# Kernel optimization log

Measured on AMD Instinct MI355X. Metric: run time of the kernel, lower is better.

The kernel has to match this reference:

```python
import jax, jax.numpy as jnp
import numpy as np

N_NODES = 100000
N_EDGES = 3200000
N_FEAT = 256
N_CLASS = 4


def setup_inputs() -> dict:
    key = jax.random.key(0)
    ks = jax.random.split(key, 8)
    x = jax.random.normal(ks[0], (N_NODES, N_FEAT), dtype=jnp.float32)
    edge_index = jax.random.randint(ks[1], (2, N_EDGES), 0, N_NODES, dtype=jnp.int64)
    def xavier(k, shape):
        fan_in, fan_out = shape
        std = np.sqrt(2.0 / (fan_in + fan_out))
        return jax.random.normal(k, shape, dtype=jnp.float32) * std
    return {
        'x': x,
        'edge_index': edge_index,
        'W_gcn': xavier(ks[2], (N_FEAT, 64)),
        'b_gcn': jnp.zeros((64,), jnp.float32),
        'W1': xavier(ks[3], (64, 32)),
        'b1': jnp.zeros((32,), jnp.float32),
        'W2': xavier(ks[4], (32, 16)),
        'b2': jnp.zeros((16,), jnp.float32),
        'W3': xavier(ks[5], (16, N_CLASS)),
        'b3': jnp.zeros((N_CLASS,), jnp.float32),
    }


def gcn_conv(x, edge_index, W, b):
    # PyG GCNConv: transform, add self-loops, symmetric normalization, scatter-add
    N = x.shape[0]
    h = x @ W  # [N, 64]
    loop = jnp.arange(N, dtype=edge_index.dtype)
    src = jnp.concatenate([edge_index[0], loop])
    dst = jnp.concatenate([edge_index[1], loop])
    deg = jax.ops.segment_sum(jnp.ones_like(dst, dtype=h.dtype), dst, num_segments=N)
    dinv = jnp.where(deg > 0, jax.lax.rsqrt(deg), 0.0)
    norm = dinv[src] * dinv[dst]  # [E+N]
    msgs = h[src] * norm[:, None]  # gather [E+N, 64]
    out = jax.ops.segment_sum(msgs, dst, num_segments=N)
    return out + b


def reference(x, edge_index, W_gcn, b_gcn, W1, b1, W2, b2, W3, b3):
    h = gcn_conv(x, edge_index, W_gcn, b_gcn)
    h = jax.nn.relu(h)          # dropout is identity in eval mode
    h = jax.nn.relu(h @ W1 + b1)
    h = jax.nn.relu(h @ W2 + b2)
    h = h @ W3 + b3
    return jax.nn.log_softmax(h, axis=1)
```

## Files before the change

kernel.cpp:

```cpp
#include <hip/hip_runtime.h>
#include <hip/hip_bf16.h>

#define NN 100000
#define NE 3200000
#define NPB 64
#define NB 1564
#define CAP 2560
#define BATCH 8192
#define NGB 1563

typedef __hip_bfloat16 bf16;
typedef __attribute__((ext_vector_type(8))) short bf16x8;
typedef __attribute__((ext_vector_type(4))) float f32x4;

__device__ __forceinline__ void fma4(float4& a, float s, const float4 w) {
  a.x = fmaf(s, w.x, a.x);
  a.y = fmaf(s, w.y, a.y);
  a.z = fmaf(s, w.z, a.z);
  a.w = fmaf(s, w.w, a.w);
}

__device__ __forceinline__ unsigned short f2b(float f) {
  unsigned u = __float_as_uint(f);
  unsigned r = ((u >> 16) & 1u) + 0x7FFFu;
  return (unsigned short)((u + r) >> 16);
}

__device__ __forceinline__ unsigned pack2(float lo, float hi) {
  return (unsigned)f2b(lo) | ((unsigned)f2b(hi) << 16);
}

__global__ void detect_k(const int* __restrict__ e, int* __restrict__ flag) {
  unsigned long long b = __ballot(e[2 * (int)threadIdx.x + 1] == 0);
  if (threadIdx.x == 0) flag[0] = (b == 0xFFFFFFFFFFFFFFFFULL) ? 1 : 0;
}

__global__ __launch_bounds__(1024) void bin_k(const void* __restrict__ eidx,
                                              const int* __restrict__ flag,
                                              int* __restrict__ bcur,
                                              int* __restrict__ buckets) {
  __shared__ int scnt[NB];
  __shared__ int lcur[NB];
  int t = threadIdx.x;
  long long e0 = (long long)blockIdx.x * BATCH;
  int m = (int)((NE - e0 < BATCH) ? (NE - e0) : BATCH);
  int isI64 = flag[0];

  for (int i = t; i < NB; i += 1024) scnt[i] = 0;
  __syncthreads();

  int ent[BATCH / 1024], bv[BATCH / 1024];
#pragma unroll
  for (int j = 0; j < BATCH / 1024; j++) {
    int idx = t + j * 1024;
    bv[j] = -1;
    if (idx < m) {
      long long i = e0 + idx;
      int s, d;
      if (isI64) {
        s = (int)((const long long*)eidx)[i];
        d = (int)((const long long*)eidx)[NE + i];
      } else {
        s = ((const int*)eidx)[i];
        d = ((const int*)eidx)[NE + i];
      }
      bv[j] = d >> 6;
      ent[j] = s | ((d & 63) << 17);
      atomicAdd(&scnt[bv[j]], 1);
    }
  }
  __syncthreads();
  for (int i = t; i < NB; i += 1024) {
    int c = scnt[i];
    lcur[i] = c ? atomicAdd(&bcur[i], c) : 0;
  }
  __syncthreads();
#pragma unroll
  for (int j = 0; j < BATCH / 1024; j++) {
    if (bv[j] >= 0) {
      int pos = atomicAdd(&lcur[bv[j]], 1);
      if (pos < CAP) buckets[(size_t)bv[j] * CAP + pos] = ent[j];
    }
  }
}

__global__ __launch_bounds__(256) void cnt_k(const int* __restrict__ buckets,
                                             const int* __restrict__ bcur,
                                             float* __restrict__ dinv,
                                             int* __restrict__ counts) {
  __shared__ int cnt[NPB];
  int b = blockIdx.x, t = threadIdx.x;
  if (t < NPB) cnt[t] = 0;
  __syncthreads();
  int m = bcur[b]; if (m > CAP) m = CAP;
  const int* bp = buckets + (size_t)b * CAP;
  for (int i = t; i < m; i += 256) atomicAdd(&cnt[(bp[i] >> 17) & 63], 1);
  __syncthreads();
  int node = b * NPB + t;
  if (t < NPB && node < NN) {
    dinv[node] = rsqrtf((float)cnt[t] + 1.0f);
    counts[node] = cnt[t];
  }
}

__global__ __launch_bounds__(256) void prep_k(const float* __restrict__ W,
                                              unsigned short* __restrict__ wh,
                                              unsigned short* __restrict__ wl) {
  int t = threadIdx.x;
#pragma unroll 4
  for (int i = 0; i < 64; i++) {
    int idx = i * 256 + t;
    int j = idx & 7;
    int lane = (idx >> 3) & 63;
    int pair = idx >> 9;
    int nf = pair & 3, kk = pair >> 2;
    int k = kk * 32 + (lane >> 4) * 8 + j;
    int n = nf * 16 + (lane & 15);
    float w = W[k * 64 + n];
    unsigned short hh = f2b(w);
    float fh = __uint_as_float((unsigned)hh << 16);
    wh[idx] = hh;
    wl[idx] = f2b(w - fh);
  }
}

__global__ __launch_bounds__(256) void gemm_k(const float* __restrict__ x,
                                              const unsigned short* __restrict__ wh,
                                              const unsigned short* __restrict__ wl,
                                              const float* __restrict__ dinv,
                                              bf16* __restrict__ h) {
  int t = threadIdx.x;
  int wv = t >> 6, l = t & 63;
  int rowbase = blockIdx.x * 64 + wv * 16;
  int arow = rowbase + (l & 15);
  if (arow >= NN) arow = NN - 1;
  const float* xrow = x + (size_t)arow * 256 + (l >> 4) * 8;

  const bf16x8* whf = (const bf16x8*)wh;
  const bf16x8* wlf = (const bf16x8*)wl;

  f32x4 acc0 = {0.f, 0.f, 0.f, 0.f};
  f32x4 acc1 = acc0, acc2 = acc0, acc3 = acc0;

#pragma unroll 1
  for (int kk = 0; kk < 8; kk++) {
    float4 xv0 = *(const float4*)(xrow + kk * 32);
    float4 xv1 = *(const float4*)(xrow + kk * 32 + 4);
    bf16x8 ah, al;
#define SP(J, F)                                                   \
    {                                                              \
      unsigned short hh_ = f2b(F);                                 \
      float fh_ = __uint_as_float((unsigned)hh_ << 16);            \
      ah[J] = (short)hh_;                                          \
      al[J] = (short)f2b((F) - fh_);                               \
    }
    SP(0, xv0.x) SP(1, xv0.y) SP(2, xv0.z) SP(3, xv0.w)
    SP(4, xv1.x) SP(5, xv1.y) SP(6, xv1.z) SP(7, xv1.w)
#undef SP
    int fb = kk * 256 + l;
    bf16x8 bh0 = whf[fb], bh1 = whf[fb + 64], bh2 = whf[fb + 128], bh3 = whf[fb + 192];
    bf16x8 bl0 = wlf[fb], bl1 = wlf[fb + 64], bl2 = wlf[fb + 128], bl3 = wlf[fb + 192];
    acc0 = __builtin_amdgcn_mfma_f32_16x16x32_bf16(ah, bh0, acc0, 0, 0, 0);
    acc1 = __builtin_amdgcn_mfma_f32_16x16x32_bf16(ah, bh1, acc1, 0, 0, 0);
    acc2 = __builtin_amdgcn_mfma_f32_16x16x32_bf16(ah, bh2, acc2, 0, 0, 0);
    acc3 = __builtin_amdgcn_mfma_f32_16x16x32_bf16(ah, bh3, acc3, 0, 0, 0);
    acc0 = __builtin_amdgcn_mfma_f32_16x16x32_bf16(ah, bl0, acc0, 0, 0, 0);
    acc1 = __builtin_amdgcn_mfma_f32_16x16x32_bf16(ah, bl1, acc1, 0, 0, 0);
    acc2 = __builtin_amdgcn_mfma_f32_16x16x32_bf16(ah, bl2, acc2, 0, 0, 0);
    acc3 = __builtin_amdgcn_mfma_f32_16x16x32_bf16(ah, bl3, acc3, 0, 0, 0);
    acc0 = __builtin_amdgcn_mfma_f32_16x16x32_bf16(al, bh0, acc0, 0, 0, 0);
    acc1 = __builtin_amdgcn_mfma_f32_16x16x32_bf16(al, bh1, acc1, 0, 0, 0);
    acc2 = __builtin_amdgcn_mfma_f32_16x16x32_bf16(al, bh2, acc2, 0, 0, 0);
    acc3 = __builtin_amdgcn_mfma_f32_16x16x32_bf16(al, bh3, acc3, 0, 0, 0);
  }

#pragma unroll
  for (int reg = 0; reg < 4; reg++) {
    int row = rowbase + (l >> 4) * 4 + reg;
    if (row < NN) {
      float dn = dinv[row];
      unsigned short* hp = (unsigned short*)h + (size_t)row * 64 + (l & 15);
      hp[0]  = f2b(acc0[reg] * dn);
      hp[16] = f2b(acc1[reg] * dn);
      hp[32] = f2b(acc2[reg] * dn);
      hp[48] = f2b(acc3[reg] * dn);
    }
  }
}

__global__ __launch_bounds__(512) void agg_k(const bf16* __restrict__ h,
                                             const int* __restrict__ buckets,
                                             const int* __restrict__ bcur,
                                             const int* __restrict__ counts,
                                             const float* __restrict__ dinv,
                                             const float* __restrict__ bg,
                                             bf16* __restrict__ hg) {
  __shared__ unsigned long long acc[NPB * 33];
  __shared__ int ents[CAP];
  int b = blockIdx.x, t = threadIdx.x;
  int node0 = b * NPB;
  int m = bcur[b]; if (m > CAP) m = CAP;
  const int* bp = buckets + (size_t)b * CAP;
  for (int i = t; i < NPB * 33; i += 512) acc[i] = 0ULL;
  for (int i = t; i < m; i += 512) ents[i] = bp[i];
  __syncthreads();
  int w = t >> 6, lane = t & 63;
  int g = lane >> 4, fl = lane & 15;
  const unsigned short* hu = (const unsigned short*)h;
#pragma unroll 4
  for (int p = w * 4 + g; p < m; p += 32) {
    int e = ents[p];
    int src = e & 0x1FFFF;
    int dl = (e >> 17) & 63;
    uint2 v = *(const uint2*)(hu + (size_t)src * 64 + fl * 4);
    unsigned i0 = (unsigned)fmaf(__uint_as_float(v.x << 16),          32768.f, 1048576.5f);
    unsigned i1 = (unsigned)fmaf(__uint_as_float(v.x & 0xFFFF0000u),  32768.f, 1048576.5f);
    unsigned i2 = (unsigned)fmaf(__uint_as_float(v.y << 16),          32768.f, 1048576.5f);
    unsigned i3 = (unsigned)fmaf(__uint_as_float(v.y & 0xFFFF0000u),  32768.f, 1048576.5f);
    unsigned long long u0 = (unsigned long long)i0 | ((unsigned long long)i1 << 32);
    unsigned long long u1 = (unsigned long long)i2 | ((unsigned long long)i3 << 32);
    unsigned long long* ap = acc + dl * 33 + fl * 2;
    atomicAdd(ap, u0);
    atomicAdd(ap + 1, u1);
  }
  __syncthreads();
  int n = t >> 3, f0 = (t & 7) * 8;
  int node = node0 + n;
  if (node < NN) {
    int cnt = counts[node];
    unsigned bias32 = (unsigned)cnt << 20;
    float dn = dinv[node];
    const unsigned long long* ap = acc + n * 33 + (f0 >> 1);
    uint4 sv = *(const uint4*)(hu + (size_t)node * 64 + f0);
    unsigned uu[4] = {sv.x, sv.y, sv.z, sv.w};
    const float* bb = bg + f0;
    unsigned short o[8];
#pragma unroll
    for (int j = 0; j < 4; j++) {
      unsigned long long u = ap[j];
      float vlo = (float)(int)((unsigned)u - bias32) * (1.f / 32768.f);
      float vhi = (float)(int)((unsigned)(u >> 32) - bias32) * (1.f / 32768.f);
      float slo = __uint_as_float(uu[j] << 16);
      float shi = __uint_as_float(uu[j] & 0xFFFF0000u);
      o[2 * j]     = f2b(fmaxf(fmaf(vlo + slo, dn, bb[2 * j]), 0.f));
      o[2 * j + 1] = f2b(fmaxf(fmaf(vhi + shi, dn, bb[2 * j + 1]), 0.f));
    }
    *(uint4*)((unsigned short*)hg + (size_t)node * 64 + f0) = *(uint4*)o;
  }
}

__global__ __launch_bounds__(256) void mlp_k(const bf16* __restrict__ hg,
                                             const float* __restrict__ W1, const float* __restrict__ b1,
                                             const float* __restrict__ W2, const float* __restrict__ b2,
                                             const float* __restrict__ W3, const float* __restrict__ b3,
                                             float* __restrict__ out) {
  __shared__ float4 sW1[512];
  __shared__ float4 sW2[128];
  __shared__ float4 sW3[16];
  __shared__ float sb1[32], sb2[16], sb3[4];
  int t = threadIdx.x;
  for (int i = t; i < 512; i += 256) sW1[i] = ((const float4*)W1)[i];
  if (t < 128) sW2[t] = ((const float4*)W2)[t];
  if (t < 16)  sW3[t] = ((const float4*)W3)[t];
  if (t < 32)  sb1[t] = b1[t];
  if (t < 16)  sb2[t] = b2[t];
  if (t < 4)   sb3[t] = b3[t];
  __syncthreads();
  int n = blockIdx.x * 256 + t;
  if (n >= NN) return;
  float xr[64];
  const uint4* hp = (const uint4*)(hg + (size_t)n * 64);
#pragma unroll
  for (int i = 0; i < 8; i++) {
    uint4 v = hp[i];
    unsigned uu[4] = {v.x, v.y, v.z, v.w};
#pragma unroll
    for (int j = 0; j < 4; j++) {
      xr[8 * i + 2 * j]     = __uint_as_float(uu[j] << 16);
      xr[8 * i + 2 * j + 1] = __uint_as_float(uu[j] & 0xFFFF0000u);
    }
  }
  float4 a1[8];
#pragma unroll
  for (int j = 0; j < 8; j++) a1[j] = make_float4(sb1[4 * j], sb1[4 * j + 1], sb1[4 * j + 2], sb1[4 * j + 3]);
#pragma unroll
  for (int f = 0; f < 64; f++) {
    float xv = xr[f];
#pragma unroll
    for (int j = 0; j < 8; j++) fma4(a1[j], xv, sW1[f * 8 + j]);
  }
  float r2[32];
#pragma unroll
  for (int j = 0; j < 8; j++) {
    r2[4 * j + 0] = fmaxf(a1[j].x, 0.f);
    r2[4 * j + 1] = fmaxf(a1[j].y, 0.f);
    r2[4 * j + 2] = fmaxf(a1[j].z, 0.f);
    r2[4 * j + 3] = fmaxf(a1[j].w, 0.f);
  }
  float4 a2[4];
#pragma unroll
  for (int j = 0; j < 4; j++) a2[j] = make_float4(sb2[4 * j], sb2[4 * j + 1], sb2[4 * j + 2], sb2[4 * j + 3]);
#pragma unroll
  for (int f = 0; f < 32; f++) {
    float xv = r2[f];
#pragma unroll
    for (int j = 0; j < 4; j++) fma4(a2[j], xv, sW2[f * 4 + j]);
  }
  float r3[16];
#pragma unroll
  for (int j = 0; j < 4; j++) {
    r3[4 * j + 0] = fmaxf(a2[j].x, 0.f);
    r3[4 * j + 1] = fmaxf(a2[j].y, 0.f);
    r3[4 * j + 2] = fmaxf(a2[j].z, 0.f);
    r3[4 * j + 3] = fmaxf(a2[j].w, 0.f);
  }
  float4 a3 = make_float4(sb3[0], sb3[1], sb3[2], sb3[3]);
#pragma unroll
  for (int f = 0; f < 16; f++) fma4(a3, r3[f], sW3[f]);
  float m = fmaxf(fmaxf(a3.x, a3.y), fmaxf(a3.z, a3.w));
  float s = expf(a3.x - m) + expf(a3.y - m) + expf(a3.z - m) + expf(a3.w - m);
  float l = m + logf(s);
  ((float4*)out)[n] = make_float4(a3.x - l, a3.y - l, a3.z - l, a3.w - l);
}

extern "C" void kernel_launch(void* const* d_in, const int* in_sizes, int n_in,
                              void* d_out, int out_size, void* d_ws, size_t ws_size,
                              hipStream_t stream) {
  const float* x  = (const float*)d_in[0];
  const void* eidx = d_in[1];
  const float* Wg = (const float*)d_in[2];
  const float* bg = (const float*)d_in[3];
  const float* W1 = (const float*)d_in[4];
  const float* b1 = (const float*)d_in[5];
  const float* W2 = (const float*)d_in[6];
  const float* b2 = (const float*)d_in[7];
  const float* W3 = (const float*)d_in[8];
  const float* b3 = (const float*)d_in[9];

  char* ws = (char*)d_ws;
  bf16*  h       = (bf16*) (ws + 0);
  bf16*  hg      = (bf16*) (ws + 12800000);
  int*   buckets = (int*)  (ws + 25600000);
  float* dinv    = (float*)(ws + 41615360);
  int*   counts  = (int*)  (ws + 42015360);
  int*   bcur    = (int*)  (ws + 42415360);
  int*   flag    = (int*)  (ws + 42421632);
  unsigned short* wh = (unsigned short*)(ws + 12800000);
  unsigned short* wl = (unsigned short*)(ws + 12800000 + 32768);

  detect_k<<<1, 64, 0, stream>>>((const int*)eidx, flag);
  hipMemsetAsync(bcur, 0, NB * sizeof(int), stream);
  bin_k<<<(NE + BATCH - 1) / BATCH, 1024, 0, stream>>>(eidx, flag, bcur, buckets);
  cnt_k<<<NB, 256, 0, stream>>>(buckets, bcur, dinv, counts);
  prep_k<<<1, 256, 0, stream>>>(Wg, wh, wl);
  gemm_k<<<NGB, 256, 0, stream>>>(x, wh, wl, dinv, h);
  agg_k<<<NB, 512, 0, stream>>>(h, buckets, bcur, counts, dinv, bg, hg);
  mlp_k<<<(NN + 255) / 256, 256, 0, stream>>>(hg, W1, b1, W2, b2, W3, b3, (float*)d_out);
}
```

Before: 171.1 us.

## Sort bucket entries per node in cnt_k and aggregate with per-node register sums

cnt_k now computes per-node offsets inside each bucket and rewrites the bucket in place as a CSR-like list of source indices grouped by destination. agg_k drops the shared-memory fixed-point 64-bit atomics and instead gives each node 8 threads that gather 16-byte bf16 row chunks and accumulate in fp32 registers, unrolled by 4. The gemm also prefetches the next x slice one iteration ahead. This removes LDS atomic contention at the cost of an extra pass over the buckets and more load imbalance from variable per-node degree. The summation order also changes from exact fixed-point integer adds to fp32 adds.

```diff
diff --git a/kernel.cpp b/kernel.cpp
--- a/kernel.cpp
+++ b/kernel.cpp
@@ -84,22 +84,44 @@
   }
 }
 
-__global__ __launch_bounds__(256) void cnt_k(const int* __restrict__ buckets,
+__global__ __launch_bounds__(256) void cnt_k(int* __restrict__ buckets,
                                              const int* __restrict__ bcur,
                                              float* __restrict__ dinv,
-                                             int* __restrict__ counts) {
+                                             int* __restrict__ counts,
+                                             int* __restrict__ offb) {
   __shared__ int cnt[NPB];
+  __shared__ int off[NPB];
+  __shared__ int lcur[NPB];
+  __shared__ int ents[CAP];
   int b = blockIdx.x, t = threadIdx.x;
   if (t < NPB) cnt[t] = 0;
   __syncthreads();
   int m = bcur[b]; if (m > CAP) m = CAP;
-  const int* bp = buckets + (size_t)b * CAP;
-  for (int i = t; i < m; i += 256) atomicAdd(&cnt[(bp[i] >> 17) & 63], 1);
-  __syncthreads();
+  int* bp = buckets + (size_t)b * CAP;
+  for (int i = t; i < m; i += 256) {
+    int e = bp[i];
+    ents[i] = e;
+    atomicAdd(&cnt[(e >> 17) & 63], 1);
+  }
+  __syncthreads();
+  if (t == 0) {
+    int s = 0;
+#pragma unroll
+    for (int i = 0; i < NPB; i++) { off[i] = s; s += cnt[i]; }
+  }
+  __syncthreads();
+  if (t < NPB) lcur[t] = off[t];
+  __syncthreads();
+  for (int i = t; i < m; i += 256) {
+    int e = ents[i];
+    int pos = atomicAdd(&lcur[(e >> 17) & 63], 1);
+    bp[pos] = e & 0x1FFFF;
+  }
   int node = b * NPB + t;
   if (t < NPB && node < NN) {
     dinv[node] = rsqrtf((float)cnt[t] + 1.0f);
     counts[node] = cnt[t];
+    offb[b * NPB + t] = off[t];
   }
 }
 
@@ -142,10 +164,14 @@
   f32x4 acc0 = {0.f, 0.f, 0.f, 0.f};
   f32x4 acc1 = acc0, acc2 = acc0, acc3 = acc0;
 
+  float4 xc0 = *(const float4*)(xrow);
+  float4 xc1 = *(const float4*)(xrow + 4);
+
 #pragma unroll 1
   for (int kk = 0; kk < 8; kk++) {
-    float4 xv0 = *(const float4*)(xrow + kk * 32);
-    float4 xv1 = *(const float4*)(xrow + kk * 32 + 4);
+    int kn = kk < 7 ? kk + 1 : 7;
+    float4 xn0 = *(const float4*)(xrow + kn * 32);
+    float4 xn1 = *(const float4*)(xrow + kn * 32 + 4);
     bf16x8 ah, al;
 #define SP(J, F)                                                   \
     {                                                              \
@@ -154,8 +180,8 @@
       ah[J] = (short)hh_;                                          \
       al[J] = (short)f2b((F) - fh_);                               \
     }
-    SP(0, xv0.x) SP(1, xv0.y) SP(2, xv0.z) SP(3, xv0.w)
-    SP(4, xv1.x) SP(5, xv1.y) SP(6, xv1.z) SP(7, xv1.w)
+    SP(0, xc0.x) SP(1, xc0.y) SP(2, xc0.z) SP(3, xc0.w)
+    SP(4, xc1.x) SP(5, xc1.y) SP(6, xc1.z) SP(7, xc1.w)
 #undef SP
     int fb = kk * 256 + l;
     bf16x8 bh0 = whf[fb], bh1 = whf[fb + 64], bh2 = whf[fb + 128], bh3 = whf[fb + 192];
@@ -172,6 +198,7 @@
     acc1 = __builtin_amdgcn_mfma_f32_16x16x32_bf16(al, bh1, acc1, 0, 0, 0);
     acc2 = __builtin_amdgcn_mfma_f32_16x16x32_bf16(al, bh2, acc2, 0, 0, 0);
     acc3 = __builtin_amdgcn_mfma_f32_16x16x32_bf16(al, bh3, acc3, 0, 0, 0);
+    xc0 = xn0; xc1 = xn1;
   }
 
 #pragma unroll
@@ -189,64 +216,61 @@
 }
 
 __global__ __launch_bounds__(512) void agg_k(const bf16* __restrict__ h,
-                                             const int* __restrict__ buckets,
-                                             const int* __restrict__ bcur,
+                                             const int* __restrict__ bsrc,
+                                             const int* __restrict__ offb,
                                              const int* __restrict__ counts,
                                              const float* __restrict__ dinv,
                                              const float* __restrict__ bg,
                                              bf16* __restrict__ hg) {
-  __shared__ unsigned long long acc[NPB * 33];
-  __shared__ int ents[CAP];
   int b = blockIdx.x, t = threadIdx.x;
-  int node0 = b * NPB;
-  int m = bcur[b]; if (m > CAP) m = CAP;
-  const int* bp = buckets + (size_t)b * CAP;
-  for (int i = t; i < NPB * 33; i += 512) acc[i] = 0ULL;
-  for (int i = t; i < m; i += 512) ents[i] = bp[i];
-  __syncthreads();
-  int w = t >> 6, lane = t & 63;
-  int g = lane >> 4, fl = lane & 15;
+  int g = t >> 3, fl = t & 7;
+  int node = b * NPB + g;
+  if (node >= NN) return;
+  int start = offb[b * NPB + g];
+  int cnt = counts[node];
+  const int* sp = bsrc + (size_t)b * CAP + start;
   const unsigned short* hu = (const unsigned short*)h;
-#pragma unroll 4
-  for (int p = w * 4 + g; p < m; p += 32) {
-    int e = ents[p];
-    int src = e & 0x1FFFF;
-    int dl = (e >> 17) & 63;
-    uint2 v = *(const uint2*)(hu + (size_t)src * 64 + fl * 4);
-    unsigned i0 = (unsigned)fmaf(__uint_as_float(v.x << 16),          32768.f, 1048576.5f);
-    unsigned i1 = (unsigned)fmaf(__uint_as_float(v.x & 0xFFFF0000u),  32768.f, 1048576.5f);
-    unsigned i2 = (unsigned)fmaf(__uint_as_float(v.y << 16),          32768.f, 1048576.5f);
-    unsigned i3 = (unsigned)fmaf(__uint_as_float(v.y & 0xFFFF0000u),  32768.f, 1048576.5f);
-    unsigned long long u0 = (unsigned long long)i0 | ((unsigned long long)i1 << 32);
-    unsigned long long u1 = (unsigned long long)i2 | ((unsigned long long)i3 << 32);
-    unsigned long long* ap = acc + dl * 33 + fl * 2;
-    atomicAdd(ap, u0);
-    atomicAdd(ap + 1, u1);
-  }
-  __syncthreads();
-  int n = t >> 3, f0 = (t & 7) * 8;
-  int node = node0 + n;
-  if (node < NN) {
-    int cnt = counts[node];
-    unsigned bias32 = (unsigned)cnt << 20;
-    float dn = dinv[node];
-    const unsigned long long* ap = acc + n * 33 + (f0 >> 1);
-    uint4 sv = *(const uint4*)(hu + (size_t)node * 64 + f0);
-    unsigned uu[4] = {sv.x, sv.y, sv.z, sv.w};
-    const float* bb = bg + f0;
-    unsigned short o[8];
-#pragma unroll
-    for (int j = 0; j < 4; j++) {
-      unsigned long long u = ap[j];
-      float vlo = (float)(int)((unsigned)u - bias32) * (1.f / 32768.f);
-      float vhi = (float)(int)((unsigned)(u >> 32) - bias32) * (1.f / 32768.f);
-      float slo = __uint_as_float(uu[j] << 16);
-      float shi = __uint_as_float(uu[j] & 0xFFFF0000u);
-      o[2 * j]     = f2b(fmaxf(fmaf(vlo + slo, dn, bb[2 * j]), 0.f));
-      o[2 * j + 1] = f2b(fmaxf(fmaf(vhi + shi, dn, bb[2 * j + 1]), 0.f));
-    }
-    *(uint4*)((unsigned short*)hg + (size_t)node * 64 + f0) = *(uint4*)o;
-  }
+
+  float a0 = 0.f, a1 = 0.f, a2 = 0.f, a3 = 0.f,
+        a4 = 0.f, a5 = 0.f, a6 = 0.f, a7 = 0.f;
+
+#define ACCV(V)                                                          \
+  {                                                                      \
+    a0 += __uint_as_float(V.x << 16); a1 += __uint_as_float(V.x & 0xFFFF0000u); \
+    a2 += __uint_as_float(V.y << 16); a3 += __uint_as_float(V.y & 0xFFFF0000u); \
+    a4 += __uint_as_float(V.z << 16); a5 += __uint_as_float(V.z & 0xFFFF0000u); \
+    a6 += __uint_as_float(V.w << 16); a7 += __uint_as_float(V.w & 0xFFFF0000u); \
+  }
+
+  int i = 0;
+  for (; i + 4 <= cnt; i += 4) {
+    int s0 = sp[i], s1 = sp[i + 1], s2 = sp[i + 2], s3 = sp[i + 3];
+    uint4 v0 = *(const uint4*)(hu + (size_t)s0 * 64 + fl * 8);
+    uint4 v1 = *(const uint4*)(hu + (size_t)s1 * 64 + fl * 8);
+    uint4 v2 = *(const uint4*)(hu + (size_t)s2 * 64 + fl * 8);
+    uint4 v3 = *(const uint4*)(hu + (size_t)s3 * 64 + fl * 8);
+    ACCV(v0) ACCV(v1) ACCV(v2) ACCV(v3)
+  }
+  for (; i < cnt; i++) {
+    int s0 = sp[i];
+    uint4 v0 = *(const uint4*)(hu + (size_t)s0 * 64 + fl * 8);
+    ACCV(v0)
+  }
+#undef ACCV
+
+  uint4 sv = *(const uint4*)(hu + (size_t)node * 64 + fl * 8);
+  float dn = dinv[node];
+  const float* bb = bg + fl * 8;
+  a0 += __uint_as_float(sv.x << 16); a1 += __uint_as_float(sv.x & 0xFFFF0000u);
+  a2 += __uint_as_float(sv.y << 16); a3 += __uint_as_float(sv.y & 0xFFFF0000u);
+  a4 += __uint_as_float(sv.z << 16); a5 += __uint_as_float(sv.z & 0xFFFF0000u);
+  a6 += __uint_as_float(sv.w << 16); a7 += __uint_as_float(sv.w & 0xFFFF0000u);
+  uint4 o;
+  o.x = pack2(fmaxf(fmaf(a0, dn, bb[0]), 0.f), fmaxf(fmaf(a1, dn, bb[1]), 0.f));
+  o.y = pack2(fmaxf(fmaf(a2, dn, bb[2]), 0.f), fmaxf(fmaf(a3, dn, bb[3]), 0.f));
+  o.z = pack2(fmaxf(fmaf(a4, dn, bb[4]), 0.f), fmaxf(fmaf(a5, dn, bb[5]), 0.f));
+  o.w = pack2(fmaxf(fmaf(a6, dn, bb[6]), 0.f), fmaxf(fmaf(a7, dn, bb[7]), 0.f));
+  *(uint4*)((unsigned short*)hg + (size_t)node * 64 + fl * 8) = o;
 }
 
 __global__ __launch_bounds__(256) void mlp_k(const bf16* __restrict__ hg,
@@ -345,15 +369,16 @@
   int*   counts  = (int*)  (ws + 42015360);
   int*   bcur    = (int*)  (ws + 42415360);
   int*   flag    = (int*)  (ws + 42421632);
+  int*   offb    = (int*)  (ws + 42421760);
   unsigned short* wh = (unsigned short*)(ws + 12800000);
   unsigned short* wl = (unsigned short*)(ws + 12800000 + 32768);
 
   detect_k<<<1, 64, 0, stream>>>((const int*)eidx, flag);
   hipMemsetAsync(bcur, 0, NB * sizeof(int), stream);
   bin_k<<<(NE + BATCH - 1) / BATCH, 1024, 0, stream>>>(eidx, flag, bcur, buckets);
-  cnt_k<<<NB, 256, 0, stream>>>(buckets, bcur, dinv, counts);
+  cnt_k<<<NB, 256, 0, stream>>>(buckets, bcur, dinv, counts, offb);
   prep_k<<<1, 256, 0, stream>>>(Wg, wh, wl);
   gemm_k<<<NGB, 256, 0, stream>>>(x, wh, wl, dinv, h);
-  agg_k<<<NB, 512, 0, stream>>>(h, buckets, bcur, counts, dinv, bg, hg);
+  agg_k<<<NB, 512, 0, stream>>>(h, buckets, offb, counts, dinv, bg, hg);
   mlp_k<<<(NN + 255) / 256, 256, 0, stream>>>(hg, W1, b1, W2, b2, W3, b3, (float*)d_out);
 }
```

Result: slower. 175.1 us (+2.3%).
